# Kernel optimization log

Hardware: AMD Instinct MI355X
Metric: run time of the kernel (lower is better)

Reference implementation:

```python
import jax, jax.numpy as jnp
import numpy as np
import itertools

F = 3          # num_sparse_features
C = 256        # num_categories
D = 64         # embedding_dim
H = 1024       # hidden_units
ND = 13        # num_dense_features
B = 16384      # batch
COMBOS = [c for r in range(2, F + 1) for c in itertools.combinations(range(F), r)]
WIDE_DIM = C * F + sum(C ** len(c) for c in COMBOS) + ND
DEEP_IN = F * D + ND


def setup_inputs() -> dict:
    key = jax.random.key(0)
    ks = jax.random.split(key, 12)
    sparse_inputs = jax.random.randint(ks[0], (B, F), 0, C, dtype=jnp.int32)
    dense_inputs = jax.random.normal(ks[1], (B, ND), dtype=jnp.float32)
    wide_w = jax.random.normal(ks[2], (WIDE_DIM,), dtype=jnp.float32) * 0.01
    wide_b = jax.random.normal(ks[3], (1,), dtype=jnp.float32) * 0.01
    emb = jax.random.normal(ks[4], (F, C, D), dtype=jnp.float32) * 0.05
    W1 = jax.random.normal(ks[5], (H, DEEP_IN), dtype=jnp.float32) / np.sqrt(DEEP_IN).astype(np.float32)
    b1 = jnp.zeros((H,), jnp.float32)
    W2 = jax.random.normal(ks[6], (H, H), dtype=jnp.float32) / np.sqrt(H).astype(np.float32)
    b2 = jnp.zeros((H,), jnp.float32)
    W3 = jax.random.normal(ks[7], (1, H), dtype=jnp.float32) / np.sqrt(H).astype(np.float32)
    b3 = jnp.zeros((1,), jnp.float32)
    return {"sparse_inputs": sparse_inputs, "dense_inputs": dense_inputs,
            "wide_w": wide_w, "wide_b": wide_b, "emb": emb,
            "W1": W1, "b1": b1, "W2": W2, "b2": b2, "W3": W3, "b3": b3}


def reference(sparse_inputs, dense_inputs, wide_w, wide_b, emb, W1, b1, W2, b2, W3, b3):
    # Wide path: one_hot(x) @ W.T  ==  gather of W columns at the hot indices.
    wide = wide_b[0]  # scalar, broadcasts to [B]
    for i in range(F):  # per-feature one-hot block, width C each
        wide = wide + wide_w[i * C + sparse_inputs[:, i]]
    off = F * C
    for combo in COMBOS:  # cross-feature one-hot blocks, width C**len(combo)
        cross = sparse_inputs[:, combo[0]]
        for j in combo[1:]:
            # faithful to source: multiplies by num_sparse_features (F), not C
            cross = cross * F + sparse_inputs[:, j]
        wide = wide + wide_w[off + cross]
        off += C ** len(combo)
    wide = wide + dense_inputs @ wide_w[off:off + ND]  # dense tail of wide linear
    wide = wide[:, None]  # [B, 1]

    # Deep path: per-feature embedding lookup -> concat -> 3-layer MLP
    embedded = jnp.concatenate([emb[i][sparse_inputs[:, i]] for i in range(F)], axis=1)  # [B, F*D]
    deep_x = jnp.concatenate([embedded, dense_inputs], axis=1)  # [B, DEEP_IN]
    h = jax.nn.relu(deep_x @ W1.T + b1)
    h = jax.nn.relu(h @ W2.T + b2)
    deep = h @ W3.T + b3  # [B, 1]

    return jax.nn.sigmoid(wide + deep)
```

## Files before the change

### kernel.cpp

```cpp
#include <hip/hip_runtime.h>
#include <stdint.h>


#define BATCH 16384
#define HDIM 1024
#define K1 256
#define DEEP_IN 205

typedef short bf16x8 __attribute__((ext_vector_type(8)));
typedef float f32x4 __attribute__((ext_vector_type(4)));
typedef uint16_t u16x8 __attribute__((ext_vector_type(8)));
typedef uint16_t u16x4 __attribute__((ext_vector_type(4)));

__device__ __forceinline__ uint16_t f2bf(float f) {
    uint32_t x;
    __builtin_memcpy(&x, &f, 4);
    uint32_t r = (x + 0x7fffu + ((x >> 16) & 1u)) >> 16;
    return (uint16_t)r;
}

__device__ __forceinline__ void async_ld16(const uint16_t* g, uint16_t* l) {
    __builtin_amdgcn_global_load_lds(
        (const __attribute__((address_space(1))) uint32_t*)g,
        (__attribute__((address_space(3))) uint32_t*)l, 16, 0, 0);
}

__global__ __launch_bounds__(256) void prep_kernel(
    const int* __restrict__ sp, const float* __restrict__ dense,
    const float* __restrict__ emb, const float* __restrict__ W1,
    const float* __restrict__ W2, const float* __restrict__ ww,
    const float* __restrict__ wb, const float* __restrict__ b3,
    uint16_t* __restrict__ embb, uint16_t* __restrict__ dtail,
    uint16_t* __restrict__ W1b, uint16_t* __restrict__ W2b,
    float* __restrict__ wide)
{
    const int bid = blockIdx.x;
    const int tid = threadIdx.x;
    if (bid < 24) {
        int k = bid * 256 + tid;
        const float* src = emb + (size_t)k * 8;
        float4 v0 = *(const float4*)src;
        float4 v1 = *(const float4*)(src + 4);
        u16x8 o;
        o[0] = f2bf(v0.x); o[1] = f2bf(v0.y); o[2] = f2bf(v0.z); o[3] = f2bf(v0.w);
        o[4] = f2bf(v1.x); o[5] = f2bf(v1.y); o[6] = f2bf(v1.z); o[7] = f2bf(v1.w);
        *(u16x8*)(embb + (size_t)k * 8) = o;
    } else if (bid < 536) {
        int idx = (bid - 24) * 256 + tid;
        int b = idx >> 3, c0 = (idx & 7) * 8;
        u16x8 o;
#pragma unroll
        for (int t = 0; t < 8; t++) {
            int c = c0 + t;
            o[t] = (c < 13) ? f2bf(dense[b * 13 + c]) : (uint16_t)0;
        }
        *(u16x8*)(dtail + (size_t)b * 64 + c0) = o;
    } else if (bid < 664) {
        int idx = (bid - 536) * 256 + tid;
        int n = idx >> 5, c0 = (idx & 31) * 8;
        u16x8 o;
#pragma unroll
        for (int t = 0; t < 8; t++) {
            int c = c0 + t;
            o[t] = (c < DEEP_IN) ? f2bf(W1[n * DEEP_IN + c]) : (uint16_t)0;
        }
        *(u16x8*)(W1b + (size_t)n * K1 + c0) = o;
    } else if (bid < 1176) {
        int k = (bid - 664) * 256 + tid;
        const float* src = W2 + (size_t)k * 8;
        float4 v0 = *(const float4*)src;
        float4 v1 = *(const float4*)(src + 4);
        u16x8 o;
        o[0] = f2bf(v0.x); o[1] = f2bf(v0.y); o[2] = f2bf(v0.z); o[3] = f2bf(v0.w);
        o[4] = f2bf(v1.x); o[5] = f2bf(v1.y); o[6] = f2bf(v1.z); o[7] = f2bf(v1.w);
        *(u16x8*)(W2b + (size_t)k * 8) = o;
    } else {
        int b = (bid - 1176) * 256 + tid;
        int s0 = sp[b * 3], s1 = sp[b * 3 + 1], s2 = sp[b * 3 + 2];
        float w = wb[0] + b3[0];
        w += ww[s0] + ww[256 + s1] + ww[512 + s2];
        w += ww[768    + s0 * 3 + s1];
        w += ww[66304  + s0 * 3 + s2];
        w += ww[131840 + s1 * 3 + s2];
        w += ww[197376 + (s0 * 3 + s1) * 3 + s2];
        const float* wd = ww + 16974592;
        float acc2 = 0.f;
#pragma unroll
        for (int j = 0; j < 13; j++) acc2 += dense[b * 13 + j] * wd[j];
        wide[b] = w + acc2;
    }
}

#define BAR8() do { asm volatile("" ::: "memory");                             \
    __builtin_amdgcn_s_barrier();                                              \
    asm volatile("" ::: "memory"); } while (0)
#define VM4() asm volatile("s_waitcnt vmcnt(4)" ::: "memory")
#define VM0() asm volatile("s_waitcnt vmcnt(0)" ::: "memory")

#define LDA8(base, msub) do {                                                  \
    _Pragma("unroll") for (int mt = 0; mt < 4; mt++) {                         \
        int ro_ = (base) + ((msub) * 64 + mt * 16) * 64;                       \
        af[mt][0] = *(const bf16x8*)&lds[ro_ + kc0];                           \
        af[mt][1] = *(const bf16x8*)&lds[ro_ + kc1];                           \
    } } while (0)

#define LDB8(dst, base, nsub) do {                                             \
    _Pragma("unroll") for (int nt = 0; nt < 2; nt++) {                         \
        int ro_ = (base) + ((nsub) * 32 + nt * 16) * 64;                       \
        dst[nt][0] = *(const bf16x8*)&lds[ro_ + kc0];                          \
        dst[nt][1] = *(const bf16x8*)&lds[ro_ + kc1];                          \
    } } while (0)

#define MM8(msub, nsub, BF) do {                                               \
    __builtin_amdgcn_s_setprio(1);                                             \
    _Pragma("unroll") for (int mt = 0; mt < 4; mt++)                           \
    _Pragma("unroll") for (int nt = 0; nt < 2; nt++) {                         \
        acc[(msub)*4+mt][(nsub)*2+nt] = __builtin_amdgcn_mfma_f32_16x16x32_bf16( \
            af[mt][0], BF[nt][0], acc[(msub)*4+mt][(nsub)*2+nt], 0, 0, 0);     \
        acc[(msub)*4+mt][(nsub)*2+nt] = __builtin_amdgcn_mfma_f32_16x16x32_bf16( \
            af[mt][1], BF[nt][1], acc[(msub)*4+mt][(nsub)*2+nt], 0, 0, 0);     \
    }                                                                          \
    __builtin_amdgcn_s_setprio(0); } while (0)

#define GEMM8_DECLS()                                                          \
    const int tid = threadIdx.x;                                               \
    const int lane = tid & 63, wave = tid >> 6;                                \
    const int wm = wave >> 2, wn = wave & 3;                                   \
    const int id = blockIdx.x;                                                 \
    const int wg = (id & 7) * 32 + (id >> 3);                                  \
    const int by = wg >> 2, bx = wg & 3;                                       \
    const int bm = by * 256, bn = bx * 256;                                    \
    const int lam = lane & 15, lad = lane >> 4;                                \
    const int sw = (lane & 7) << 4;                                            \
    const int kc0 = ((lad * 16) ^ sw) >> 1;                                    \
    const int kc1 = ((64 + lad * 16) ^ sw) >> 1;                               \
    const int aBE = wm * 8192 + lam * 64;                                      \
    const int aBO = aBE + 16384;                                               \
    const int bBE = 32768 + (wn >> 1) * 8192 + ((wn & 1) * 64 + lam) * 64;     \
    const int bBO = bBE + 16384;                                               \
    const int trow = tid >> 3;                                                 \
    const int csel = ((tid & 7) ^ (trow & 7)) << 3;

#define GEMM8_MAIN()                                                           \
    f32x4 acc[8][4];                                                           \
    _Pragma("unroll") for (int i = 0; i < 8; i++)                              \
        _Pragma("unroll") for (int j = 0; j < 4; j++) acc[i][j] = (f32x4)0.f;  \
    bf16x8 af[4][2], bf0[2][2], bf1[2][2];                                     \
    const int NT = K >> 6;                                                     \
    const int NI = K >> 7;                                                     \
    STG8A(0, 0, 0);     STG8A(0, 1, 0);                                        \
    STG8B(32768, 0, 0); STG8B(32768, 1, 0);                                    \
    STG8B(49152, 0, 64); STG8B(49152, 1, 64);                                  \
    VM4();                                                                     \
    BAR8();                                                                    \
    for (int it = 0; it < NI; ++it) {                                          \
        const int k1 = (2 * it + 1) * 64;                                      \
        const int t2 = 2 * it + 2, t3 = 2 * it + 3;                            \
        const int k2 = (t2 < NT ? t2 : 0) * 64;                                \
        const int k3 = (t3 < NT ? t3 : 0) * 64;                                \
        LDA8(aBE, 0); LDB8(bf0, bBE, 0); STG8A(16384, 0, k1);                  \
        BAR8(); MM8(0, 0, bf0); BAR8();                                        \
        LDB8(bf1, bBE, 1); STG8A(16384, 1, k1);                                \
        BAR8(); MM8(0, 1, bf1); BAR8();                                        \
        LDA8(aBE, 1); STG8B(32768, 0, k2);                                     \
        BAR8(); MM8(1, 1, bf1); BAR8();                                        \
        STG8B(32768, 1, k2);                                                   \
        BAR8(); MM8(1, 0, bf0); VM4(); BAR8();                                 \
        LDA8(aBO, 0); LDB8(bf0, bBO, 0); STG8A(0, 0, k2);                      \
        BAR8(); MM8(0, 0, bf0); BAR8();                                        \
        LDB8(bf1, bBO, 1); STG8A(0, 1, k2);                                    \
        BAR8(); MM8(0, 1, bf1); BAR8();                                        \
        LDA8(aBO, 1); STG8B(49152, 0, k3);                                     \
        BAR8(); MM8(1, 1, bf1); BAR8();                                        \
        STG8B(49152, 1, k3);                                                   \
        BAR8(); MM8(1, 0, bf0); VM4(); BAR8();                                 \
    }

#define ASRC1(pkv, h2, kt) ((kt) < 192                                         \
    ? (embb + (((kt) >> 6) << 14)                                              \
            + ((int)(((pkv) >> (((kt) >> 6) << 3)) & 255u) << 6) + csel)       \
    : (dtail + (size_t)(b0 + (h2) * 64) * 64 + csel))

#define STG8A(regoff, h, kt) do {                                              \
    async_ld16(ASRC1(PK##h##_0, 2*(h), kt),                                    \
               &lds[(regoff) + (h) * 8192 + wave * 512]);                      \
    async_ld16(ASRC1(PK##h##_1, 2*(h)+1, kt),                                  \
               &lds[(regoff) + (h) * 8192 + 4096 + wave * 512]);               \
} while (0)

#define STG8B(regoff, h, kt) do {                                              \
    const uint16_t* g_ = bRow + (size_t)((h) * 128) * (size_t)K + (kt);        \
    async_ld16(g_, &lds[(regoff) + (h) * 8192 + wave * 512]);                  \
    async_ld16(g_ + (size_t)64 * (size_t)K,                                    \
               &lds[(regoff) + (h) * 8192 + 4096 + wave * 512]);               \
} while (0)

__global__ __launch_bounds__(512, 2) void gemm1_8(
    const int* __restrict__ sp, const uint16_t* __restrict__ embb,
    const uint16_t* __restrict__ dtail, const uint16_t* __restrict__ Bw,
    const float* __restrict__ bias, uint16_t* __restrict__ C)
{
    __shared__ __align__(16) uint16_t lds[65536];
    GEMM8_DECLS()
    const int K = K1;
    const int b0 = bm + trow;
    const uint32_t PK0_0 = (uint32_t)sp[(b0      ) * 3] |
                           ((uint32_t)sp[(b0      ) * 3 + 1] << 8) |
                           ((uint32_t)sp[(b0      ) * 3 + 2] << 16);
    const uint32_t PK0_1 = (uint32_t)sp[(b0 +  64) * 3] |
                           ((uint32_t)sp[(b0 +  64) * 3 + 1] << 8) |
                           ((uint32_t)sp[(b0 +  64) * 3 + 2] << 16);
    const uint32_t PK1_0 = (uint32_t)sp[(b0 + 128) * 3] |
                           ((uint32_t)sp[(b0 + 128) * 3 + 1] << 8) |
                           ((uint32_t)sp[(b0 + 128) * 3 + 2] << 16);
    const uint32_t PK1_1 = (uint32_t)sp[(b0 + 192) * 3] |
                           ((uint32_t)sp[(b0 + 192) * 3 + 1] << 8) |
                           ((uint32_t)sp[(b0 + 192) * 3 + 2] << 16);
    const int prow = 4 * (trow & 15) + (trow >> 4);
    const uint16_t* bRow = Bw + (size_t)(bn + prow) * K + csel;
    VM0();
    GEMM8_MAIN()

    float bv[4];
#pragma unroll
    for (int jn = 0; jn < 4; jn++) bv[jn] = bias[bn + wn * 64 + 4 * lam + jn];
#pragma unroll
    for (int im = 0; im < 8; im++) {
#pragma unroll
        for (int r = 0; r < 4; r++) {
            int m = bm + wm * 128 + im * 16 + lad * 4 + r;
            u16x4 o;
#pragma unroll
            for (int jn = 0; jn < 4; jn++)
                o[jn] = f2bf(fmaxf(acc[im][jn][r] + bv[jn], 0.f));
            *(u16x4*)&C[(size_t)m * HDIM + bn + wn * 64 + 4 * lam] = o;
        }
    }
}

#undef STG8A
#undef STG8B

#define STG8A(regoff, h, kt) do {                                              \
    const uint16_t* g_ = aRow + (size_t)((h) * 128) * (size_t)K + (kt);        \
    async_ld16(g_, &lds[(regoff) + (h) * 8192 + wave * 512]);                  \
    async_ld16(g_ + (size_t)64 * (size_t)K,                                    \
               &lds[(regoff) + (h) * 8192 + 4096 + wave * 512]);               \
} while (0)

#define STG8B(regoff, h, kt) do {                                              \
    const uint16_t* g_ = bRow + (size_t)((h) * 128) * (size_t)K + (kt);        \
    async_ld16(g_, &lds[(regoff) + (h) * 8192 + wave * 512]);                  \
    async_ld16(g_ + (size_t)64 * (size_t)K,                                    \
               &lds[(regoff) + (h) * 8192 + 4096 + wave * 512]);               \
} while (0)

__global__ __launch_bounds__(512, 2) void gemm_fused8(
    const uint16_t* __restrict__ A, const uint16_t* __restrict__ Bw,
    const float* __restrict__ bias, const float* __restrict__ W3,
    float* __restrict__ outacc, int M, int N, int K)
{
    __shared__ __align__(16) uint16_t lds[65536];
    GEMM8_DECLS()
    const uint16_t* aRow = A + (size_t)(bm + trow) * K + csel;
    const uint16_t* bRow = Bw + (size_t)(bn + trow) * K + csel;
    GEMM8_MAIN()

    float bv[4], w3v[4];
#pragma unroll
    for (int jn = 0; jn < 4; jn++) {
        int n = bn + wn * 64 + jn * 16 + lam;
        bv[jn] = bias[n];
        w3v[jn] = W3[n];
    }
#pragma unroll
    for (int im = 0; im < 8; im++) {
#pragma unroll
        for (int r = 0; r < 4; r++) {
            float pt = 0.f;
#pragma unroll
            for (int jn = 0; jn < 4; jn++)
                pt += fmaxf(acc[im][jn][r] + bv[jn], 0.f) * w3v[jn];
            pt += __shfl_xor(pt, 1);
            pt += __shfl_xor(pt, 2);
            pt += __shfl_xor(pt, 4);
            pt += __shfl_xor(pt, 8);
            if (lam == 0) {
                int m = bm + wm * 128 + im * 16 + lad * 4 + r;
                atomicAdd(&outacc[m], pt);
            }
        }
    }
}

#undef STG8A
#undef STG8B

__global__ __launch_bounds__(256) void sigmoid_kernel(
    const float* __restrict__ outacc, float* __restrict__ out)
{
    int b = blockIdx.x * 256 + threadIdx.x;
    out[b] = 1.f / (1.f + __expf(-outacc[b]));
}

extern "C" void kernel_launch(void* const* d_in, const int* in_sizes, int n_in,
                              void* d_out, int out_size, void* d_ws, size_t ws_size,
                              hipStream_t stream) {
    const int*   sp    = (const int*)d_in[0];
    const float* dense = (const float*)d_in[1];
    const float* ww    = (const float*)d_in[2];
    const float* wb    = (const float*)d_in[3];
    const float* emb   = (const float*)d_in[4];
    const float* W1    = (const float*)d_in[5];
    const float* b1    = (const float*)d_in[6];
    const float* W2    = (const float*)d_in[7];
    const float* b2    = (const float*)d_in[8];
    const float* W3    = (const float*)d_in[9];
    const float* b3    = (const float*)d_in[10];
    float* out = (float*)d_out;

    char* ws = (char*)d_ws;
    float*    wide  = (float*)ws;
    uint16_t* embb  = (uint16_t*)(ws + 65536);
    uint16_t* dtail = (uint16_t*)(ws + 163840);
    uint16_t* W1b   = (uint16_t*)(ws + 2260992);
    uint16_t* W2b   = (uint16_t*)(ws + 2785280);
    uint16_t* h1    = (uint16_t*)(ws + 4882432);

    prep_kernel<<<1240, 256, 0, stream>>>(
        sp, dense, emb, W1, W2, ww, wb, b3, embb, dtail, W1b, W2b, wide);
    gemm1_8<<<256, 512, 0, stream>>>(
        sp, embb, dtail, W1b, b1, h1);
    gemm_fused8<<<256, 512, 0, stream>>>(
        h1, W2b, b2, W3, wide, BATCH, HDIM, HDIM);
    sigmoid_kernel<<<BATCH / 256, 256, 0, stream>>>(wide, out);
}
```

Before: 159.2 us.

## Shrink second-GEMM tile to 256x128 with new double-buffered pipeline

The fused second GEMM moves from 256x256 tiles on 256 blocks to 256x128 tiles on 512 blocks. The K loop is rewritten with its own staging, LDS read and MFMA macros, using a different buffer layout, vmcnt(2) waits, and a smaller 96KB LDS allocation. The goal is more blocks than CUs on the mi355x, to fill the machine better and cut tail imbalance. In exchange, arithmetic intensity per tile drops, A-tile reloads double, and atomic adds into the output accumulator increase.

```diff
diff --git a/kernel.cpp b/kernel.cpp
--- a/kernel.cpp
+++ b/kernel.cpp
@@ -95,6 +95,7 @@
     __builtin_amdgcn_s_barrier();                                              \
     asm volatile("" ::: "memory"); } while (0)
 #define VM4() asm volatile("s_waitcnt vmcnt(4)" ::: "memory")
+#define VM2() asm volatile("s_waitcnt vmcnt(2)" ::: "memory")
 #define VM0() asm volatile("s_waitcnt vmcnt(0)" ::: "memory")
 
 #define LDA8(base, msub) do {                                                  \
@@ -241,37 +242,103 @@
 #undef STG8A
 #undef STG8B
 
-#define STG8A(regoff, h, kt) do {                                              \
-    const uint16_t* g_ = aRow + (size_t)((h) * 128) * (size_t)K + (kt);        \
-    async_ld16(g_, &lds[(regoff) + (h) * 8192 + wave * 512]);                  \
-    async_ld16(g_ + (size_t)64 * (size_t)K,                                    \
-               &lds[(regoff) + (h) * 8192 + 4096 + wave * 512]);               \
-} while (0)
-
-#define STG8B(regoff, h, kt) do {                                              \
-    const uint16_t* g_ = bRow + (size_t)((h) * 128) * (size_t)K + (kt);        \
-    async_ld16(g_, &lds[(regoff) + (h) * 8192 + wave * 512]);                  \
-    async_ld16(g_ + (size_t)64 * (size_t)K,                                    \
-               &lds[(regoff) + (h) * 8192 + 4096 + wave * 512]);               \
-} while (0)
+#define STA3(reg, c, kt) async_ld16(                                           \
+    aRow + (size_t)((c) * 64) * (size_t)K + (kt),                              \
+    &lds[(reg) + (c) * 4096 + wave * 512])
+
+#define STB3(reg, c, kt) async_ld16(                                           \
+    bRow + (size_t)((c) * 64) * (size_t)K + (kt),                              \
+    &lds[(reg) + (c) * 4096 + wave * 512])
+
+#define LDAH(reg, msub) do {                                                   \
+    _Pragma("unroll") for (int mt = 0; mt < 4; mt++) {                         \
+        int ro_ = (reg) + aRd + ((msub) * 64 + mt * 16) * 64;                  \
+        af[mt][0] = *(const bf16x8*)&lds[ro_ + kc0];                           \
+        af[mt][1] = *(const bf16x8*)&lds[ro_ + kc1];                           \
+    } } while (0)
+
+#define LDBH(reg) do {                                                         \
+    _Pragma("unroll") for (int nt = 0; nt < 2; nt++) {                         \
+        int ro_ = (reg) + bRd + nt * 1024;                                     \
+        bf[nt][0] = *(const bf16x8*)&lds[ro_ + kc0];                           \
+        bf[nt][1] = *(const bf16x8*)&lds[ro_ + kc1];                           \
+    } } while (0)
+
+#define MMH(msub) do {                                                         \
+    __builtin_amdgcn_s_setprio(1);                                             \
+    _Pragma("unroll") for (int mt = 0; mt < 4; mt++)                           \
+    _Pragma("unroll") for (int nt = 0; nt < 2; nt++) {                         \
+        acc[(msub)*4+mt][nt] = __builtin_amdgcn_mfma_f32_16x16x32_bf16(        \
+            af[mt][0], bf[nt][0], acc[(msub)*4+mt][nt], 0, 0, 0);              \
+        acc[(msub)*4+mt][nt] = __builtin_amdgcn_mfma_f32_16x16x32_bf16(        \
+            af[mt][1], bf[nt][1], acc[(msub)*4+mt][nt], 0, 0, 0);              \
+    }                                                                          \
+    __builtin_amdgcn_s_setprio(0); } while (0)
 
 __global__ __launch_bounds__(512, 2) void gemm_fused8(
     const uint16_t* __restrict__ A, const uint16_t* __restrict__ Bw,
     const float* __restrict__ bias, const float* __restrict__ W3,
     float* __restrict__ outacc, int M, int N, int K)
 {
-    __shared__ __align__(16) uint16_t lds[65536];
-    GEMM8_DECLS()
+    __shared__ __align__(16) uint16_t lds[49152];
+    const int tid = threadIdx.x;
+    const int lane = tid & 63, wave = tid >> 6;
+    const int wm = wave >> 2, wn = wave & 3;
+    const int id = blockIdx.x;
+    const int wg = (id & 7) * 64 + (id >> 3);
+    const int by = wg >> 3, bx = wg & 7;
+    const int bm = by * 256, bn = bx * 128;
+    const int lam = lane & 15, lad = lane >> 4;
+    const int sw = (lane & 7) << 4;
+    const int kc0 = ((lad * 16) ^ sw) >> 1;
+    const int kc1 = ((64 + lad * 16) ^ sw) >> 1;
+    const int aRd = (wm * 128 + lam) * 64;
+    const int bRd = (wn * 32 + lam) * 64;
+    const int trow = tid >> 3;
+    const int csel = ((tid & 7) ^ (trow & 7)) << 3;
     const uint16_t* aRow = A + (size_t)(bm + trow) * K + csel;
     const uint16_t* bRow = Bw + (size_t)(bn + trow) * K + csel;
-    GEMM8_MAIN()
-
-    float bv[4], w3v[4];
-#pragma unroll
-    for (int jn = 0; jn < 4; jn++) {
-        int n = bn + wn * 64 + jn * 16 + lam;
-        bv[jn] = bias[n];
-        w3v[jn] = W3[n];
+
+    f32x4 acc[8][2];
+#pragma unroll
+    for (int i = 0; i < 8; i++)
+#pragma unroll
+        for (int j = 0; j < 2; j++) acc[i][j] = (f32x4)0.f;
+    bf16x8 af[4][2], bf[2][2];
+    const int NT = K >> 6;
+    const int NI = K >> 7;
+
+    STA3(0, 0, 0); STA3(0, 1, 0); STA3(0, 2, 0); STA3(0, 3, 0);
+    STB3(32768, 0, 0); STB3(32768, 1, 0);
+    STB3(40960, 0, 64); STB3(40960, 1, 64);
+    VM2();
+    BAR8();
+
+    for (int it = 0; it < NI; ++it) {
+        const int ktO = (it << 7) + 64;
+        const int tE = 2 * it + 2, tO = 2 * it + 3;
+        const int ktNE = (tE < NT ? tE : 0) << 6;
+        const int ktNO = (tO < NT ? tO : 0) << 6;
+        LDAH(0, 0); LDBH(32768);
+        STA3(16384, 0, ktO); STA3(16384, 1, ktO); STA3(16384, 2, ktO);
+        BAR8(); MMH(0); BAR8();
+        LDAH(0, 1);
+        STA3(16384, 3, ktO); STB3(32768, 0, ktNE); STB3(32768, 1, ktNE);
+        BAR8(); MMH(1); VM2(); BAR8();
+        LDAH(16384, 0); LDBH(40960);
+        STA3(0, 0, ktNE); STA3(0, 1, ktNE); STA3(0, 2, ktNE);
+        BAR8(); MMH(0); BAR8();
+        LDAH(16384, 1);
+        STA3(0, 3, ktNE); STB3(40960, 0, ktNO); STB3(40960, 1, ktNO);
+        BAR8(); MMH(1); VM2(); BAR8();
+    }
+
+    float bv[2], w3v[2];
+#pragma unroll
+    for (int nt = 0; nt < 2; nt++) {
+        int n = bn + wn * 32 + nt * 16 + lam;
+        bv[nt] = bias[n];
+        w3v[nt] = W3[n];
     }
 #pragma unroll
     for (int im = 0; im < 8; im++) {
@@ -279,8 +346,8 @@
         for (int r = 0; r < 4; r++) {
             float pt = 0.f;
 #pragma unroll
-            for (int jn = 0; jn < 4; jn++)
-                pt += fmaxf(acc[im][jn][r] + bv[jn], 0.f) * w3v[jn];
+            for (int nt = 0; nt < 2; nt++)
+                pt += fmaxf(acc[im][nt][r] + bv[nt], 0.f) * w3v[nt];
             pt += __shfl_xor(pt, 1);
             pt += __shfl_xor(pt, 2);
             pt += __shfl_xor(pt, 4);
@@ -293,8 +360,11 @@
     }
 }
 
-#undef STG8A
-#undef STG8B
+#undef STA3
+#undef STB3
+#undef LDAH
+#undef LDBH
+#undef MMH
 
 __global__ __launch_bounds__(256) void sigmoid_kernel(
     const float* __restrict__ outacc, float* __restrict__ out)
@@ -331,7 +401,7 @@
         sp, dense, emb, W1, W2, ww, wb, b3, embb, dtail, W1b, W2b, wide);
     gemm1_8<<<256, 512, 0, stream>>>(
         sp, embb, dtail, W1b, b1, h1);
-    gemm_fused8<<<256, 512, 0, stream>>>(
+    gemm_fused8<<<512, 512, 0, stream>>>(
         h1, W2b, b2, W3, wide, BATCH, HDIM, HDIM);
     sigmoid_kernel<<<BATCH / 256, 256, 0, stream>>>(wide, out);
 }
```

Result: slower. 175.5 us (+10.2%).
